# Performance work log

Measured on AMD Instinct MI355X. Metric: run time of the kernel, lower is better.

The kernel has to match this reference:

```python
import jax, jax.numpy as jnp
import numpy as np
from jax import lax

STATE_DIM = 8
HIDDEN = 32
SEED_H = 8
SEED_W = 8
N_ITER = 64


def setup_inputs() -> dict:
    key = jax.random.key(0)
    k_seed, k_w1, k_w2, k_wp = jax.random.split(key, 4)
    seed = jax.random.normal(k_seed, (1, STATE_DIM, SEED_H, SEED_W), dtype=jnp.float32) * 0.1
    # Conv2d(state_dim, hidden, 3) weights, kaiming-uniform-ish init
    fan1 = STATE_DIM * 9
    W1 = jax.random.uniform(k_w1, (HIDDEN, STATE_DIM, 3, 3), dtype=jnp.float32,
                            minval=-1.0, maxval=1.0) / np.sqrt(fan1).astype(np.float32)
    b1 = jnp.zeros((HIDDEN,), dtype=jnp.float32)
    # Conv2d(hidden, state_dim, 1)
    fan2 = HIDDEN
    W2 = jax.random.uniform(k_w2, (STATE_DIM, HIDDEN, 1, 1), dtype=jnp.float32,
                            minval=-1.0, maxval=1.0) / np.sqrt(fan2).astype(np.float32)
    b2 = jnp.zeros((STATE_DIM,), dtype=jnp.float32)
    # Linear(state_dim, 1)
    Wp = jax.random.uniform(k_wp, (1, STATE_DIM), dtype=jnp.float32,
                            minval=-1.0, maxval=1.0) / np.sqrt(STATE_DIM).astype(np.float32)
    bp = jnp.zeros((1,), dtype=jnp.float32)
    return {"seed": seed, "W1": W1, "b1": b1, "W2": W2, "b2": b2,
            "Wp": Wp, "bp": bp, "rows": 1024, "cols": 1024}


def _conv(x, w, b):
    y = lax.conv_general_dilated(x, w, window_strides=(1, 1), padding="SAME",
                                 dimension_numbers=("NCHW", "OIHW", "NCHW"))
    return y + b[None, :, None, None]


def reference(seed, W1, b1, W2, b2, Wp, bp, rows, cols):
    # F.interpolate(seed, (rows, cols), mode='bilinear', align_corners=False)
    x = jax.image.resize(seed, (1, STATE_DIM, rows, cols), method="bilinear")
    keys = jax.random.split(jax.random.key(42), N_ITER)

    def step(x, k):
        h = jax.nn.gelu(_conv(x, W1, b1), approximate=False)
        dx = _conv(h, W2, b2) * 0.1
        mask = (jax.random.uniform(k, (1, 1, rows, cols)) > 0.5).astype(x.dtype)
        return x + dx * mask, None

    x, _ = lax.scan(step, x, keys)
    # project: Linear(state_dim, 1) over channel axis -> [rows, cols]
    out = jnp.einsum("chw,oc->hw", x[0], Wp) + bp[0]
    return out
```

## Files before the change

kernel.cpp:

```cpp
#include <hip/hip_runtime.h>
#include <cstdint>
#include <cstddef>


#define HH 1024
#define WW 1024
#define SD 8
#define TX 32
#define TY 16
#define NA 612
#define SWA 36

typedef _Float16 f16x8 __attribute__((ext_vector_type(8)));
typedef float f32x4 __attribute__((ext_vector_type(4)));
typedef uint32_t u32x2 __attribute__((ext_vector_type(2)));
typedef uint32_t u32x4 __attribute__((ext_vector_type(4)));

__host__ __device__ inline uint32_t rotl32(uint32_t x, int n) {
  return (x << n) | (x >> (32 - n));
}

__host__ __device__ inline void tf2x32(uint32_t k0, uint32_t k1,
                                       uint32_t x0, uint32_t x1,
                                       uint32_t& o0, uint32_t& o1) {
  uint32_t ks0 = k0, ks1 = k1, ks2 = k0 ^ k1 ^ 0x1BD11BDAu;
  x0 += ks0; x1 += ks1;
#define TFR(r) { x0 += x1; x1 = rotl32(x1, (r)); x1 ^= x0; }
  TFR(13) TFR(15) TFR(26) TFR(6)  x0 += ks1; x1 += ks2 + 1u;
  TFR(17) TFR(29) TFR(16) TFR(24) x0 += ks2; x1 += ks0 + 2u;
  TFR(13) TFR(15) TFR(26) TFR(6)  x0 += ks0; x1 += ks1 + 3u;
  TFR(17) TFR(29) TFR(16) TFR(24) x0 += ks1; x1 += ks2 + 4u;
  TFR(13) TFR(15) TFR(26) TFR(6)  x0 += ks2; x1 += ks0 + 5u;
#undef TFR
  o0 = x0; o1 = x1;
}

__device__ inline float gelu_fast(float x) {
  const float s = x * x;
  const float z = x * fmaf(0.0713548162f, s, 1.5957691216f);
  const float e = __expf(z);
  const float t = __builtin_amdgcn_rcpf(1.0f + e);
  return fmaf(-x, t, x);
}

__global__ void init_kernel(const float* __restrict__ seed, _Float16* __restrict__ dst) {
  int p = blockIdx.x * blockDim.x + threadIdx.x;
  if (p >= HH * WW) return;
  int y = p >> 10, x = p & 1023;
  float fy = (y + 0.5f) * (8.0f / HH) - 0.5f;
  float fx = (x + 0.5f) * (8.0f / WW) - 0.5f;
  int y0 = (int)floorf(fy); float wy = fy - (float)y0;
  int x0 = (int)floorf(fx); float wx = fx - (float)x0;
  int y0c = min(max(y0, 0), 7), y1c = min(max(y0 + 1, 0), 7);
  int x0c = min(max(x0, 0), 7), x1c = min(max(x0 + 1, 0), 7);
  f16x8 v;
#pragma unroll
  for (int c = 0; c < SD; ++c) {
    const float* s = seed + c * 64;
    float v00 = s[y0c * 8 + x0c], v01 = s[y0c * 8 + x1c];
    float v10 = s[y1c * 8 + x0c], v11 = s[y1c * 8 + x1c];
    float v0 = v00 + (v01 - v00) * wx;
    float v1 = v10 + (v11 - v10) * wx;
    v[c] = (_Float16)(v0 + (v1 - v0) * wy);
  }
  *(f16x8*)(dst + (size_t)p * 8) = v;
}

__global__ void prep_kernel(const float* __restrict__ W1, const float* __restrict__ W2,
                            _Float16* __restrict__ w1f, _Float16* __restrict__ w2f) {
  int tid = threadIdx.x;
  for (int i = tid; i < 2 * 3 * 64; i += 256) {
    int nt = i / 192, rem = i % 192;
    int kc = rem / 64, lane = rem % 64;
    int ir = lane & 15;
    int ch = (ir >> 2) * 8 + (ir & 3) + nt * 4;
    int tap = kc * 4 + (lane >> 4);
#pragma unroll
    for (int j = 0; j < 8; ++j) {
      float v = (tap < 9) ? W1[(ch * SD + j) * 9 + tap] : 0.0f;
      w1f[i * 8 + j] = (_Float16)v;
    }
  }
  if (tid < 64) {
    int n = tid & 15, qk = tid >> 4;
#pragma unroll
    for (int j = 0; j < 8; ++j) {
      float v = (n < 8) ? W2[n * 32 + qk * 8 + j] : 0.0f;
      w2f[tid * 8 + j] = (_Float16)v;
    }
  }
}

__global__ __launch_bounds__(256) void step2_kernel(
    const _Float16* __restrict__ src, _Float16* __restrict__ dst,
    const _Float16* __restrict__ w1f, const _Float16* __restrict__ w2f,
    const float* __restrict__ b1, const float* __restrict__ b2,
    uint32_t k0a, uint32_t k1a, uint32_t k0b, uint32_t k1b) {
  __shared__ _Float16 tileA[20 * SWA * SD];
  __shared__ _Float16 dxw[NA * SD];

  const int tid = threadIdx.x;
  const int bx = blockIdx.x;
  const int lane = tid & 63, w = tid >> 6;
  const int m = lane & 15, q = lane >> 4;

  f16x8 af[2][3];
#pragma unroll
  for (int nt = 0; nt < 2; ++nt)
#pragma unroll
    for (int kc = 0; kc < 3; ++kc)
      af[nt][kc] = *(const f16x8*)(w1f + ((nt * 3 + kc) * 64 + lane) * 8);
  const f16x8 w2fr = *(const f16x8*)(w2f + lane * 8);
  const f32x4 b1q0 = *(const f32x4*)(b1 + q * 8);
  const f32x4 b1q1 = *(const f32x4*)(b1 + q * 8 + 4);
  const f32x4 b2q = *(const f32x4*)(b2 + (q & 1) * 4);

  int off[3];
#pragma unroll
  for (int kc = 0; kc < 3; ++kc) {
    int t = kc * 4 + q; if (t > 8) t = 0;
    off[kc] = ((t / 3) * SWA + (t % 3)) * 8;
  }

#pragma unroll 1
  for (int it2 = 0; it2 < 2; ++it2) {
    const int by = blockIdx.y + it2 * 32;
    if (it2) __syncthreads();

    for (int i = tid; i < 20 * SWA; i += 256) {
      int ly = i / SWA, lx = i - (i / SWA) * SWA;
      int gy = by * TY + ly - 2, gx = bx * TX + lx - 2;
      u32x4 v = {0u, 0u, 0u, 0u};
      if ((unsigned)gy < HH && (unsigned)gx < WW)
        v = *(const u32x4*)(src + (size_t)(gy * WW + gx) * 8);
      *(u32x4*)&tileA[i * 8] = v;
    }

    _Float16 maskB[2];
#pragma unroll
    for (int half = 0; half < 2; ++half) {
      const int p = w * 128 + half * 64 + lane;
      const uint32_t gp = (uint32_t)((by * TY + (p >> 5)) * WW + bx * TX + (p & 31));
      uint32_t r0, r1;
      tf2x32(k0b, k1b, 0u, gp, r0, r1);
      maskB[half] = (((r0 ^ r1) >> 9) > 0x400000u) ? (_Float16)0.1f : (_Float16)0.0f;
    }
    __syncthreads();

    for (int gi = 0; gi < 10; ++gi) {
      const int G = w * 10 + gi;
      const int p = G * 16 + m;
      const int r = (p * 241) >> 13;
      const int c = p - r * 34;
      const int base = (r * SWA + c) * 8;
      f32x4 acc0 = b1q0, acc1 = b1q1;
#pragma unroll
      for (int kc = 0; kc < 3; ++kc) {
        const f16x8 bfrag = *(const f16x8*)&tileA[base + off[kc]];
        acc0 = __builtin_amdgcn_mfma_f32_16x16x32_f16(af[0][kc], bfrag, acc0, 0, 0, 0);
        acc1 = __builtin_amdgcn_mfma_f32_16x16x32_f16(af[1][kc], bfrag, acc1, 0, 0, 0);
      }
      u32x4 a2d;
      {
        float g0 = gelu_fast(acc0[0]), g1 = gelu_fast(acc0[1]);
        float g2 = gelu_fast(acc0[2]), g3 = gelu_fast(acc0[3]);
        float g4 = gelu_fast(acc1[0]), g5 = gelu_fast(acc1[1]);
        float g6 = gelu_fast(acc1[2]), g7 = gelu_fast(acc1[3]);
        a2d[0] = __builtin_bit_cast(uint32_t, __builtin_amdgcn_cvt_pkrtz(g0, g1));
        a2d[1] = __builtin_bit_cast(uint32_t, __builtin_amdgcn_cvt_pkrtz(g2, g3));
        a2d[2] = __builtin_bit_cast(uint32_t, __builtin_amdgcn_cvt_pkrtz(g4, g5));
        a2d[3] = __builtin_bit_cast(uint32_t, __builtin_amdgcn_cvt_pkrtz(g6, g7));
      }
      const f16x8 hB = __builtin_bit_cast(f16x8, a2d);
      f32x4 acc2 = b2q;
      acc2 = __builtin_amdgcn_mfma_f32_16x16x32_f16(w2fr, hB, acc2, 0, 0, 0);
      if (q < 2 && p < NA) {
        u32x2 dd;
        dd[0] = __builtin_bit_cast(uint32_t, __builtin_amdgcn_cvt_pkrtz(acc2[0], acc2[1]));
        dd[1] = __builtin_bit_cast(uint32_t, __builtin_amdgcn_cvt_pkrtz(acc2[2], acc2[3]));
        *(u32x2*)&dxw[p * 8 + q * 4] = dd;
      }
    }
    __syncthreads();

#pragma unroll
    for (int k = 0; k < 3; ++k) {
      const int p = tid + k * 256;
      if (p < NA) {
        const int r = (p * 241) >> 13;
        const int c = p - r * 34;
        const int gy = by * TY + r - 1, gx = bx * TX + c - 1;
        _Float16 mk = (_Float16)0.0f;
        if (((unsigned)gy < HH) && ((unsigned)gx < WW)) {
          uint32_t r0, r1;
          tf2x32(k0a, k1a, 0u, (uint32_t)(gy * WW + gx), r0, r1);
          mk = (((r0 ^ r1) >> 9) > 0x400000u) ? (_Float16)0.1f : (_Float16)0.0f;
        }
        _Float16* xp = &tileA[((r + 1) * SWA + (c + 1)) * 8];
        const f16x8 xi = *(const f16x8*)xp;
        const f16x8 dx = *(const f16x8*)&dxw[p * 8];
        const f16x8 mk8 = {mk, mk, mk, mk, mk, mk, mk, mk};
        const f16x8 xo = dx * mk8 + xi;
        *(f16x8*)xp = xo;
      }
    }
    __syncthreads();

    for (int gi = 0; gi < 8; ++gi) {
      const int G = w * 8 + gi;
      const int p = G * 16 + m;
      const int r = p >> 5, c = p & 31;
      const int base = ((r + 1) * SWA + (c + 1)) * 8;
      f32x4 acc0 = b1q0, acc1 = b1q1;
#pragma unroll
      for (int kc = 0; kc < 3; ++kc) {
        const f16x8 bfrag = *(const f16x8*)&tileA[base + off[kc]];
        acc0 = __builtin_amdgcn_mfma_f32_16x16x32_f16(af[0][kc], bfrag, acc0, 0, 0, 0);
        acc1 = __builtin_amdgcn_mfma_f32_16x16x32_f16(af[1][kc], bfrag, acc1, 0, 0, 0);
      }
      u32x4 a2d;
      {
        float g0 = gelu_fast(acc0[0]), g1 = gelu_fast(acc0[1]);
        float g2 = gelu_fast(acc0[2]), g3 = gelu_fast(acc0[3]);
        float g4 = gelu_fast(acc1[0]), g5 = gelu_fast(acc1[1]);
        float g6 = gelu_fast(acc1[2]), g7 = gelu_fast(acc1[3]);
        a2d[0] = __builtin_bit_cast(uint32_t, __builtin_amdgcn_cvt_pkrtz(g0, g1));
        a2d[1] = __builtin_bit_cast(uint32_t, __builtin_amdgcn_cvt_pkrtz(g2, g3));
        a2d[2] = __builtin_bit_cast(uint32_t, __builtin_amdgcn_cvt_pkrtz(g4, g5));
        a2d[3] = __builtin_bit_cast(uint32_t, __builtin_amdgcn_cvt_pkrtz(g6, g7));
      }
      const f16x8 hB = __builtin_bit_cast(f16x8, a2d);
      f32x4 acc2 = b2q;
      acc2 = __builtin_amdgcn_mfma_f32_16x16x32_f16(w2fr, hB, acc2, 0, 0, 0);
      if (q < 2) {
        u32x2 dd;
        dd[0] = __builtin_bit_cast(uint32_t, __builtin_amdgcn_cvt_pkrtz(acc2[0], acc2[1]));
        dd[1] = __builtin_bit_cast(uint32_t, __builtin_amdgcn_cvt_pkrtz(acc2[2], acc2[3]));
        *(u32x2*)&dxw[p * 8 + q * 4] = dd;
      }
    }

#pragma unroll
    for (int half = 0; half < 2; ++half) {
      const int pw = half * 64 + lane;
      const int p = w * 128 + pw;
      const int py = p >> 5, px = p & 31;
      const uint32_t gp = (uint32_t)((by * TY + py) * WW + bx * TX + px);
      const _Float16 mk = maskB[half];
      const f16x8 xi = *(const f16x8*)&tileA[((py + 2) * SWA + (px + 2)) * 8];
      const f16x8 dx = *(const f16x8*)&dxw[p * 8];
      const f16x8 mk8 = {mk, mk, mk, mk, mk, mk, mk, mk};
      const f16x8 xo = dx * mk8 + xi;
      *(f16x8*)(dst + (size_t)gp * 8) = xo;
    }
  }
}

__global__ void proj_kernel(const _Float16* __restrict__ x,
                            const float* __restrict__ Wp,
                            const float* __restrict__ bp,
                            float* __restrict__ out) {
  int p = blockIdx.x * blockDim.x + threadIdx.x;
  if (p >= HH * WW) return;
  const f16x8 xv = *(const f16x8*)(x + (size_t)p * 8);
  float acc = bp[0];
#pragma unroll
  for (int c = 0; c < SD; ++c) acc = fmaf((float)xv[c], Wp[c], acc);
  out[p] = acc;
}

extern "C" void kernel_launch(void* const* d_in, const int* in_sizes, int n_in,
                              void* d_out, int out_size, void* d_ws, size_t ws_size,
                              hipStream_t stream) {
  (void)in_sizes; (void)n_in; (void)out_size; (void)ws_size;
  const float* seed = (const float*)d_in[0];
  const float* W1   = (const float*)d_in[1];
  const float* b1   = (const float*)d_in[2];
  const float* W2   = (const float*)d_in[3];
  const float* b2   = (const float*)d_in[4];
  const float* Wp   = (const float*)d_in[5];
  const float* bp   = (const float*)d_in[6];
  float* out  = (float*)d_out;
  _Float16* buf0 = (_Float16*)d_ws;
  _Float16* buf1 = buf0 + (size_t)SD * HH * WW;
  _Float16* w1f  = buf1 + (size_t)SD * HH * WW;
  _Float16* w2f  = w1f + 2 * 3 * 64 * 8;

  uint32_t ka[64], kb[64];
  for (int i = 0; i < 64; ++i) tf2x32(0u, 42u, 0u, (uint32_t)i, ka[i], kb[i]);

  hipLaunchKernelGGL(prep_kernel, dim3(1), dim3(256), 0, stream, W1, W2, w1f, w2f);
  hipLaunchKernelGGL(init_kernel, dim3((HH * WW) / 256), dim3(256), 0, stream, seed, buf0);

  dim3 grid(WW / TX, 32);
  _Float16* s = buf0; _Float16* d = buf1;
  for (int i = 0; i < 64; i += 2) {
    hipLaunchKernelGGL(step2_kernel, grid, dim3(256), 0, stream,
                       s, d, w1f, w2f, b1, b2, ka[i], kb[i], ka[i + 1], kb[i + 1]);
    _Float16* t = s; s = d; d = t;
  }
  hipLaunchKernelGGL(proj_kernel, dim3((HH * WW) / 256), dim3(256), 0, stream,
                     s, Wp, bp, out);
}
```

Measured before the change: 1.389 ms.

## Use 32x32 tiles with 512 threads and ping-pong LDS buffers in fused two-step kernel

Each block now covers a 32x32 output tile with 512 threads instead of looping twice over 32x16 tiles with 256 threads. This lowers the halo recompute ratio for the fused two-step stencil. The intermediate state is written into the dx buffer and the second step's dx into tileA, so the two LDS arrays are reused as ping-pong buffers and a barrier is removed. The mask hash is computed inline at store time. LDS per block grows to about 39 KB, which may limit how many blocks fit per CU.

```diff
diff --git a/kernel.cpp b/kernel.cpp
--- a/kernel.cpp
+++ b/kernel.cpp
@@ -7,8 +7,10 @@
 #define WW 1024
 #define SD 8
 #define TX 32
-#define TY 16
-#define NA 612
+#define TY 32
+#define DA 34
+#define NA 1156
+#define NGA 73
 #define SWA 36
 
 typedef _Float16 f16x8 __attribute__((ext_vector_type(8)));
@@ -91,16 +93,16 @@
   }
 }
 
-__global__ __launch_bounds__(256) void step2_kernel(
+__global__ __launch_bounds__(512, 8) void step2_kernel(
     const _Float16* __restrict__ src, _Float16* __restrict__ dst,
     const _Float16* __restrict__ w1f, const _Float16* __restrict__ w2f,
     const float* __restrict__ b1, const float* __restrict__ b2,
     uint32_t k0a, uint32_t k1a, uint32_t k0b, uint32_t k1b) {
-  __shared__ _Float16 tileA[20 * SWA * SD];
+  __shared__ _Float16 tileA[SWA * SWA * SD];
   __shared__ _Float16 dxw[NA * SD];
 
   const int tid = threadIdx.x;
-  const int bx = blockIdx.x;
+  const int bx = blockIdx.x, by = blockIdx.y;
   const int lane = tid & 63, w = tid >> 6;
   const int m = lane & 15, q = lane >> 4;
 
@@ -115,144 +117,132 @@
   const f32x4 b1q1 = *(const f32x4*)(b1 + q * 8 + 4);
   const f32x4 b2q = *(const f32x4*)(b2 + (q & 1) * 4);
 
-  int off[3];
+  int offA[3], offB[3];
 #pragma unroll
   for (int kc = 0; kc < 3; ++kc) {
     int t = kc * 4 + q; if (t > 8) t = 0;
-    off[kc] = ((t / 3) * SWA + (t % 3)) * 8;
-  }
-
-#pragma unroll 1
-  for (int it2 = 0; it2 < 2; ++it2) {
-    const int by = blockIdx.y + it2 * 32;
-    if (it2) __syncthreads();
-
-    for (int i = tid; i < 20 * SWA; i += 256) {
-      int ly = i / SWA, lx = i - (i / SWA) * SWA;
-      int gy = by * TY + ly - 2, gx = bx * TX + lx - 2;
-      u32x4 v = {0u, 0u, 0u, 0u};
-      if ((unsigned)gy < HH && (unsigned)gx < WW)
-        v = *(const u32x4*)(src + (size_t)(gy * WW + gx) * 8);
-      *(u32x4*)&tileA[i * 8] = v;
-    }
-
-    _Float16 maskB[2];
-#pragma unroll
-    for (int half = 0; half < 2; ++half) {
-      const int p = w * 128 + half * 64 + lane;
-      const uint32_t gp = (uint32_t)((by * TY + (p >> 5)) * WW + bx * TX + (p & 31));
-      uint32_t r0, r1;
-      tf2x32(k0b, k1b, 0u, gp, r0, r1);
-      maskB[half] = (((r0 ^ r1) >> 9) > 0x400000u) ? (_Float16)0.1f : (_Float16)0.0f;
-    }
-    __syncthreads();
-
-    for (int gi = 0; gi < 10; ++gi) {
-      const int G = w * 10 + gi;
-      const int p = G * 16 + m;
+    offA[kc] = ((t / 3) * SWA + (t % 3)) * 8;
+    offB[kc] = ((t / 3) * DA + (t % 3)) * 8;
+  }
+
+  for (int i = tid; i < SWA * SWA; i += 512) {
+    int ly = i / SWA, lx = i - (i / SWA) * SWA;
+    int gy = by * TY + ly - 2, gx = bx * TX + lx - 2;
+    u32x4 v = {0u, 0u, 0u, 0u};
+    if ((unsigned)gy < HH && (unsigned)gx < WW)
+      v = *(const u32x4*)(src + (size_t)(gy * WW + gx) * 8);
+    *(u32x4*)&tileA[i * 8] = v;
+  }
+  __syncthreads();
+
+  for (int gi = 0; gi < 10; ++gi) {
+    const int G = w + 8 * gi;
+    if (G >= NGA) break;
+    const int p = G * 16 + m;
+    const int r = (p * 241) >> 13;
+    const int c = p - r * DA;
+    const int base = (r * SWA + c) * 8;
+    f32x4 acc0 = b1q0, acc1 = b1q1;
+#pragma unroll
+    for (int kc = 0; kc < 3; ++kc) {
+      const f16x8 bfrag = *(const f16x8*)&tileA[base + offA[kc]];
+      acc0 = __builtin_amdgcn_mfma_f32_16x16x32_f16(af[0][kc], bfrag, acc0, 0, 0, 0);
+      acc1 = __builtin_amdgcn_mfma_f32_16x16x32_f16(af[1][kc], bfrag, acc1, 0, 0, 0);
+    }
+    u32x4 a2d;
+    {
+      float g0 = gelu_fast(acc0[0]), g1 = gelu_fast(acc0[1]);
+      float g2 = gelu_fast(acc0[2]), g3 = gelu_fast(acc0[3]);
+      float g4 = gelu_fast(acc1[0]), g5 = gelu_fast(acc1[1]);
+      float g6 = gelu_fast(acc1[2]), g7 = gelu_fast(acc1[3]);
+      a2d[0] = __builtin_bit_cast(uint32_t, __builtin_amdgcn_cvt_pkrtz(g0, g1));
+      a2d[1] = __builtin_bit_cast(uint32_t, __builtin_amdgcn_cvt_pkrtz(g2, g3));
+      a2d[2] = __builtin_bit_cast(uint32_t, __builtin_amdgcn_cvt_pkrtz(g4, g5));
+      a2d[3] = __builtin_bit_cast(uint32_t, __builtin_amdgcn_cvt_pkrtz(g6, g7));
+    }
+    const f16x8 hB = __builtin_bit_cast(f16x8, a2d);
+    f32x4 acc2 = b2q;
+    acc2 = __builtin_amdgcn_mfma_f32_16x16x32_f16(w2fr, hB, acc2, 0, 0, 0);
+    if (q < 2 && p < NA) {
+      u32x2 dd;
+      dd[0] = __builtin_bit_cast(uint32_t, __builtin_amdgcn_cvt_pkrtz(acc2[0], acc2[1]));
+      dd[1] = __builtin_bit_cast(uint32_t, __builtin_amdgcn_cvt_pkrtz(acc2[2], acc2[3]));
+      *(u32x2*)&dxw[p * 8 + q * 4] = dd;
+    }
+  }
+
+#pragma unroll
+  for (int j = 0; j < 3; ++j) {
+    const int G = w + 8 * (j * 4 + (lane >> 4));
+    const int p = G * 16 + m;
+    if (G < NGA && p < NA) {
       const int r = (p * 241) >> 13;
-      const int c = p - r * 34;
-      const int base = (r * SWA + c) * 8;
-      f32x4 acc0 = b1q0, acc1 = b1q1;
-#pragma unroll
-      for (int kc = 0; kc < 3; ++kc) {
-        const f16x8 bfrag = *(const f16x8*)&tileA[base + off[kc]];
-        acc0 = __builtin_amdgcn_mfma_f32_16x16x32_f16(af[0][kc], bfrag, acc0, 0, 0, 0);
-        acc1 = __builtin_amdgcn_mfma_f32_16x16x32_f16(af[1][kc], bfrag, acc1, 0, 0, 0);
+      const int c = p - r * DA;
+      const int gy = by * TY + r - 1, gx = bx * TX + c - 1;
+      _Float16 mk = (_Float16)0.0f;
+      if (((unsigned)gy < HH) && ((unsigned)gx < WW)) {
+        uint32_t r0, r1;
+        tf2x32(k0a, k1a, 0u, (uint32_t)(gy * WW + gx), r0, r1);
+        mk = (((r0 ^ r1) >> 9) > 0x400000u) ? (_Float16)0.1f : (_Float16)0.0f;
       }
-      u32x4 a2d;
-      {
-        float g0 = gelu_fast(acc0[0]), g1 = gelu_fast(acc0[1]);
-        float g2 = gelu_fast(acc0[2]), g3 = gelu_fast(acc0[3]);
-        float g4 = gelu_fast(acc1[0]), g5 = gelu_fast(acc1[1]);
-        float g6 = gelu_fast(acc1[2]), g7 = gelu_fast(acc1[3]);
-        a2d[0] = __builtin_bit_cast(uint32_t, __builtin_amdgcn_cvt_pkrtz(g0, g1));
-        a2d[1] = __builtin_bit_cast(uint32_t, __builtin_amdgcn_cvt_pkrtz(g2, g3));
-        a2d[2] = __builtin_bit_cast(uint32_t, __builtin_amdgcn_cvt_pkrtz(g4, g5));
-        a2d[3] = __builtin_bit_cast(uint32_t, __builtin_amdgcn_cvt_pkrtz(g6, g7));
-      }
-      const f16x8 hB = __builtin_bit_cast(f16x8, a2d);
-      f32x4 acc2 = b2q;
-      acc2 = __builtin_amdgcn_mfma_f32_16x16x32_f16(w2fr, hB, acc2, 0, 0, 0);
-      if (q < 2 && p < NA) {
-        u32x2 dd;
-        dd[0] = __builtin_bit_cast(uint32_t, __builtin_amdgcn_cvt_pkrtz(acc2[0], acc2[1]));
-        dd[1] = __builtin_bit_cast(uint32_t, __builtin_amdgcn_cvt_pkrtz(acc2[2], acc2[3]));
-        *(u32x2*)&dxw[p * 8 + q * 4] = dd;
-      }
-    }
-    __syncthreads();
-
-#pragma unroll
-    for (int k = 0; k < 3; ++k) {
-      const int p = tid + k * 256;
-      if (p < NA) {
-        const int r = (p * 241) >> 13;
-        const int c = p - r * 34;
-        const int gy = by * TY + r - 1, gx = bx * TX + c - 1;
-        _Float16 mk = (_Float16)0.0f;
-        if (((unsigned)gy < HH) && ((unsigned)gx < WW)) {
-          uint32_t r0, r1;
-          tf2x32(k0a, k1a, 0u, (uint32_t)(gy * WW + gx), r0, r1);
-          mk = (((r0 ^ r1) >> 9) > 0x400000u) ? (_Float16)0.1f : (_Float16)0.0f;
-        }
-        _Float16* xp = &tileA[((r + 1) * SWA + (c + 1)) * 8];
-        const f16x8 xi = *(const f16x8*)xp;
-        const f16x8 dx = *(const f16x8*)&dxw[p * 8];
-        const f16x8 mk8 = {mk, mk, mk, mk, mk, mk, mk, mk};
-        const f16x8 xo = dx * mk8 + xi;
-        *(f16x8*)xp = xo;
-      }
-    }
-    __syncthreads();
-
-    for (int gi = 0; gi < 8; ++gi) {
-      const int G = w * 8 + gi;
-      const int p = G * 16 + m;
-      const int r = p >> 5, c = p & 31;
-      const int base = ((r + 1) * SWA + (c + 1)) * 8;
-      f32x4 acc0 = b1q0, acc1 = b1q1;
-#pragma unroll
-      for (int kc = 0; kc < 3; ++kc) {
-        const f16x8 bfrag = *(const f16x8*)&tileA[base + off[kc]];
-        acc0 = __builtin_amdgcn_mfma_f32_16x16x32_f16(af[0][kc], bfrag, acc0, 0, 0, 0);
-        acc1 = __builtin_amdgcn_mfma_f32_16x16x32_f16(af[1][kc], bfrag, acc1, 0, 0, 0);
-      }
-      u32x4 a2d;
-      {
-        float g0 = gelu_fast(acc0[0]), g1 = gelu_fast(acc0[1]);
-        float g2 = gelu_fast(acc0[2]), g3 = gelu_fast(acc0[3]);
-        float g4 = gelu_fast(acc1[0]), g5 = gelu_fast(acc1[1]);
-        float g6 = gelu_fast(acc1[2]), g7 = gelu_fast(acc1[3]);
-        a2d[0] = __builtin_bit_cast(uint32_t, __builtin_amdgcn_cvt_pkrtz(g0, g1));
-        a2d[1] = __builtin_bit_cast(uint32_t, __builtin_amdgcn_cvt_pkrtz(g2, g3));
-        a2d[2] = __builtin_bit_cast(uint32_t, __builtin_amdgcn_cvt_pkrtz(g4, g5));
-        a2d[3] = __builtin_bit_cast(uint32_t, __builtin_amdgcn_cvt_pkrtz(g6, g7));
-      }
-      const f16x8 hB = __builtin_bit_cast(f16x8, a2d);
-      f32x4 acc2 = b2q;
-      acc2 = __builtin_amdgcn_mfma_f32_16x16x32_f16(w2fr, hB, acc2, 0, 0, 0);
-      if (q < 2) {
-        u32x2 dd;
-        dd[0] = __builtin_bit_cast(uint32_t, __builtin_amdgcn_cvt_pkrtz(acc2[0], acc2[1]));
-        dd[1] = __builtin_bit_cast(uint32_t, __builtin_amdgcn_cvt_pkrtz(acc2[2], acc2[3]));
-        *(u32x2*)&dxw[p * 8 + q * 4] = dd;
-      }
-    }
-
-#pragma unroll
-    for (int half = 0; half < 2; ++half) {
-      const int pw = half * 64 + lane;
-      const int p = w * 128 + pw;
-      const int py = p >> 5, px = p & 31;
-      const uint32_t gp = (uint32_t)((by * TY + py) * WW + bx * TX + px);
-      const _Float16 mk = maskB[half];
-      const f16x8 xi = *(const f16x8*)&tileA[((py + 2) * SWA + (px + 2)) * 8];
+      const f16x8 xi = *(const f16x8*)&tileA[((r + 1) * SWA + (c + 1)) * 8];
       const f16x8 dx = *(const f16x8*)&dxw[p * 8];
       const f16x8 mk8 = {mk, mk, mk, mk, mk, mk, mk, mk};
       const f16x8 xo = dx * mk8 + xi;
-      *(f16x8*)(dst + (size_t)gp * 8) = xo;
-    }
+      *(f16x8*)&dxw[p * 8] = xo;
+    }
+  }
+  __syncthreads();
+
+  for (int gi = 0; gi < 8; ++gi) {
+    const int G = w + 8 * gi;
+    const int p = G * 16 + m;
+    const int r = p >> 5, c = p & 31;
+    const int base = (r * DA + c) * 8;
+    f32x4 acc0 = b1q0, acc1 = b1q1;
+#pragma unroll
+    for (int kc = 0; kc < 3; ++kc) {
+      const f16x8 bfrag = *(const f16x8*)&dxw[base + offB[kc]];
+      acc0 = __builtin_amdgcn_mfma_f32_16x16x32_f16(af[0][kc], bfrag, acc0, 0, 0, 0);
+      acc1 = __builtin_amdgcn_mfma_f32_16x16x32_f16(af[1][kc], bfrag, acc1, 0, 0, 0);
+    }
+    u32x4 a2d;
+    {
+      float g0 = gelu_fast(acc0[0]), g1 = gelu_fast(acc0[1]);
+      float g2 = gelu_fast(acc0[2]), g3 = gelu_fast(acc0[3]);
+      float g4 = gelu_fast(acc1[0]), g5 = gelu_fast(acc1[1]);
+      float g6 = gelu_fast(acc1[2]), g7 = gelu_fast(acc1[3]);
+      a2d[0] = __builtin_bit_cast(uint32_t, __builtin_amdgcn_cvt_pkrtz(g0, g1));
+      a2d[1] = __builtin_bit_cast(uint32_t, __builtin_amdgcn_cvt_pkrtz(g2, g3));
+      a2d[2] = __builtin_bit_cast(uint32_t, __builtin_amdgcn_cvt_pkrtz(g4, g5));
+      a2d[3] = __builtin_bit_cast(uint32_t, __builtin_amdgcn_cvt_pkrtz(g6, g7));
+    }
+    const f16x8 hB = __builtin_bit_cast(f16x8, a2d);
+    f32x4 acc2 = b2q;
+    acc2 = __builtin_amdgcn_mfma_f32_16x16x32_f16(w2fr, hB, acc2, 0, 0, 0);
+    if (q < 2) {
+      u32x2 dd;
+      dd[0] = __builtin_bit_cast(uint32_t, __builtin_amdgcn_cvt_pkrtz(acc2[0], acc2[1]));
+      dd[1] = __builtin_bit_cast(uint32_t, __builtin_amdgcn_cvt_pkrtz(acc2[2], acc2[3]));
+      *(u32x2*)&tileA[p * 8 + q * 4] = dd;
+    }
+  }
+
+#pragma unroll
+  for (int j = 0; j < 2; ++j) {
+    const int G = w + 8 * (j * 4 + (lane >> 4));
+    const int p = G * 16 + m;
+    const int r = p >> 5, c = p & 31;
+    const int pA = (r + 1) * DA + (c + 1);
+    const uint32_t gp = (uint32_t)((by * TY + r) * WW + bx * TX + c);
+    uint32_t r0, r1;
+    tf2x32(k0b, k1b, 0u, gp, r0, r1);
+    const _Float16 mk = (((r0 ^ r1) >> 9) > 0x400000u) ? (_Float16)0.1f : (_Float16)0.0f;
+    const f16x8 xB = *(const f16x8*)&dxw[pA * 8];
+    const f16x8 dx = *(const f16x8*)&tileA[p * 8];
+    const f16x8 mk8 = {mk, mk, mk, mk, mk, mk, mk, mk};
+    const f16x8 xo = dx * mk8 + xB;
+    *(f16x8*)(dst + (size_t)gp * 8) = xo;
   }
 }
 
@@ -292,10 +282,10 @@
   hipLaunchKernelGGL(prep_kernel, dim3(1), dim3(256), 0, stream, W1, W2, w1f, w2f);
   hipLaunchKernelGGL(init_kernel, dim3((HH * WW) / 256), dim3(256), 0, stream, seed, buf0);
 
-  dim3 grid(WW / TX, 32);
+  dim3 grid(WW / TX, HH / TY);
   _Float16* s = buf0; _Float16* d = buf1;
   for (int i = 0; i < 64; i += 2) {
-    hipLaunchKernelGGL(step2_kernel, grid, dim3(256), 0, stream,
+    hipLaunchKernelGGL(step2_kernel, grid, dim3(512), 0, stream,
                        s, d, w1f, w2f, b1, b2, ka[i], kb[i], ka[i + 1], kb[i + 1]);
     _Float16* t = s; s = d; d = t;
   }
```

New measurement: 1.340 ms (median of 2 runs). -3.5%, faster.
